# Performance work log

Measured on AMD Instinct MI355X. Metric: run time of the kernel, lower is better.

The kernel has to match this reference:

```python
import jax, jax.numpy as jnp
import numpy as np

B, T, C, HS = 64, 256, 2048, 128


def setup_inputs() -> dict:
    key = jax.random.key(0)
    k1, k2, k3, k4 = jax.random.split(key, 4)
    x = jax.random.normal(k1, (B, T, C), dtype=jnp.float32)
    # Dense(head_size, use_bias=False) kernels, scaled like glorot-ish init
    Wk = jax.random.normal(k2, (C, HS), dtype=jnp.float32) * (C ** -0.5)
    Wq = jax.random.normal(k3, (C, HS), dtype=jnp.float32) * (C ** -0.5)
    Wv = jax.random.normal(k4, (C, HS), dtype=jnp.float32) * (C ** -0.5)
    return {"x": x, "Wk": Wk, "Wq": Wq, "Wv": Wv}


def reference(x, Wk, Wq, Wv):
    Bn, Tn, Cn = x.shape
    k = jnp.einsum("btc,ch->bth", x, Wk)
    q = jnp.einsum("btc,ch->bth", x, Wq)
    v = jnp.einsum("btc,ch->bth", x, Wv)
    # faithful to source: scores = k @ q^T, scaled by C**-0.5 (input dim!)
    scores = jnp.einsum("bth,bsh->bts", k, q) * (Cn ** -0.5)
    causal = jnp.tril(jnp.ones((Tn, Tn), dtype=bool))  # [T, T]
    scores = jnp.where(causal, scores, -jnp.inf)
    weights = jax.nn.softmax(scores, axis=-1)
    return jnp.einsum("bts,bsh->bth", weights, v)
```

## Files before the change

### kernel.cpp

```cpp
#include <hip/hip_runtime.h>
#include <hip/hip_bf16.h>
#include <cstdint>
#include <cstddef>

#define B_  64
#define T_  256
#define C_  2048
#define HS_ 128
#define N_  384

typedef __bf16 bf16x8 __attribute__((ext_vector_type(8)));
typedef float  floatx4 __attribute__((ext_vector_type(4)));

__device__ __forceinline__ unsigned short f2bf_rne(float f) {
  union { float f; unsigned int u; } v; v.f = f;
  unsigned int r = v.u + 0x7fffu + ((v.u >> 16) & 1u);
  return (unsigned short)(r >> 16);
}
__device__ __forceinline__ unsigned short f2bf(float f) {
  union { float f; unsigned int u; } v; v.f = f;
  return (unsigned short)((v.u + 0x8000u) >> 16);
}

__global__ __launch_bounds__(256) void wt_kernel(
    const float* __restrict__ Wk, const float* __restrict__ Wq,
    const float* __restrict__ Wv, unsigned short* __restrict__ Wt) {
  __shared__ float tile[32][33];
  const int w  = blockIdx.z;
  const int c0 = blockIdx.x * 32;
  const int h0 = blockIdx.y * 32;
  const float* W = (w == 0) ? Wk : (w == 1) ? Wq : Wv;
  const int tx = threadIdx.x & 31, ty = threadIdx.x >> 5;
#pragma unroll
  for (int i = 0; i < 32; i += 8)
    tile[ty + i][tx] = W[(size_t)(c0 + ty + i) * HS_ + h0 + tx];
  __syncthreads();
#pragma unroll
  for (int i = 0; i < 32; i += 8) {
    int hh = ty + i, cc = tx;
    Wt[(size_t)(w * HS_ + h0 + hh) * C_ + c0 + cc] = f2bf_rne(tile[cc][hh]);
  }
}

__global__ __launch_bounds__(256, 2) void qkv_gemm(
    const float* __restrict__ X, const unsigned short* __restrict__ Wt,
    unsigned short* __restrict__ kqv, unsigned short* __restrict__ vT) {
  __shared__ unsigned short As[2][64 * 32];

  const int tid  = threadIdx.x;
  const int wave = tid >> 6, lane = tid & 63;
  const int quad = lane >> 4, l16 = lane & 15;

  const int m0    = blockIdx.x * 64;
  const int nbase = blockIdx.y * 192 + wave * 48;

  const int arow  = tid >> 3;
  const int acol4 = (tid & 7) * 4;

  const float* Xr0 = X + (size_t)(m0 + arow) * C_ + acol4;
  const float* Xr1 = X + (size_t)(m0 + arow + 32) * C_ + acol4;

  const unsigned short* Bp[3];
#pragma unroll
  for (int nt = 0; nt < 3; ++nt)
    Bp[nt] = Wt + (size_t)(nbase + nt * 16 + l16) * C_ + quad * 8;

  float4 a0 = *(const float4*)(Xr0);
  float4 a1 = *(const float4*)(Xr1);
  bf16x8 bcur[3];
#pragma unroll
  for (int nt = 0; nt < 3; ++nt) bcur[nt] = *(const bf16x8*)(Bp[nt]);

  floatx4 acc[4][3] = {};

  for (int k = 0; k < 64; ++k) {
    const int cur = k & 1;
    ushort4 u0, u1;
    u0.x = f2bf(a0.x); u0.y = f2bf(a0.y); u0.z = f2bf(a0.z); u0.w = f2bf(a0.w);
    u1.x = f2bf(a1.x); u1.y = f2bf(a1.y); u1.z = f2bf(a1.z); u1.w = f2bf(a1.w);
    *(ushort4*)&As[cur][arow * 32 + acol4]        = u0;
    *(ushort4*)&As[cur][(arow + 32) * 32 + acol4] = u1;
    __syncthreads();

    bf16x8 bnxt[3] = {bcur[0], bcur[1], bcur[2]};
    if (k < 63) {
      const int kn = (k + 1) * 32;
      a0 = *(const float4*)(Xr0 + kn);
      a1 = *(const float4*)(Xr1 + kn);
#pragma unroll
      for (int nt = 0; nt < 3; ++nt)
        bnxt[nt] = *(const bf16x8*)(Bp[nt] + kn);
    }

    bf16x8 af[4];
#pragma unroll
    for (int mt = 0; mt < 4; ++mt)
      af[mt] = *(const bf16x8*)&As[cur][(mt * 16 + l16) * 32 + quad * 8];
#pragma unroll
    for (int mt = 0; mt < 4; ++mt)
#pragma unroll
      for (int nt = 0; nt < 3; ++nt)
        acc[mt][nt] = __builtin_amdgcn_mfma_f32_16x16x32_bf16(
            af[mt], bcur[nt], acc[mt][nt], 0, 0, 0);
#pragma unroll
    for (int nt = 0; nt < 3; ++nt) bcur[nt] = bnxt[nt];
  }

#pragma unroll
  for (int mt = 0; mt < 4; ++mt)
#pragma unroll
    for (int nt = 0; nt < 3; ++nt) {
      const int n = nbase + nt * 16 + l16;
      const bool isv = (nbase + nt * 16) >= 256;
#pragma unroll
      for (int r = 0; r < 4; ++r) {
        int m = m0 + mt * 16 + quad * 4 + r;
        unsigned short us = f2bf(acc[mt][nt][r]);
        kqv[(size_t)m * N_ + n] = us;
        if (isv) {
          int bb = m >> 8, tt = m & 255;
          vT[(size_t)bb * HS_ * T_ + (size_t)(n - 256) * T_ + tt] = us;
        }
      }
    }
}

__global__ __launch_bounds__(256) void attn_kernel(
    const unsigned short* __restrict__ kqv, const unsigned short* __restrict__ vT,
    float* __restrict__ out) {
  constexpr int PS = 264;
  __shared__ unsigned short P[16 * PS];
  __shared__ float rsumw[4][16];

  const int tid  = threadIdx.x;
  const int p    = tid >> 6;
  const int lane = tid & 63;
  const int quad = lane >> 4, l16 = lane & 15;
  const int tt = blockIdx.x;
  const int b  = blockIdx.y;
  const int t0 = tt * 16;
  const float scale = 0.022097086912079612f;
  const unsigned short* kq = kqv + (size_t)b * T_ * N_;

  bf16x8 kf[4];
#pragma unroll
  for (int ks = 0; ks < 4; ++ks)
    kf[ks] = *(const bf16x8*)&kq[(size_t)(t0 + l16) * N_ + ks * 32 + quad * 8];

  if ((tt & 1) == 0 && p == ((tt + 1) & 3)) {
#pragma unroll
    for (int r = 0; r < 4; ++r)
      P[(quad * 4 + r) * PS + (tt + 1) * 16 + l16] = 0;
  }

  float rsum[4] = {0.f, 0.f, 0.f, 0.f};
  for (int st = p; st <= tt; st += 4) {
    floatx4 a = {};
#pragma unroll
    for (int ks = 0; ks < 4; ++ks) {
      bf16x8 qf = *(const bf16x8*)&kq[(size_t)(st * 16 + l16) * N_ + HS_ +
                                      ks * 32 + quad * 8];
      a = __builtin_amdgcn_mfma_f32_16x16x32_bf16(kf[ks], qf, a, 0, 0, 0);
    }
    const int scol = st * 16 + l16;
#pragma unroll
    for (int r = 0; r < 4; ++r) {
      int trow = t0 + quad * 4 + r;
      float pv = (scol <= trow) ? __expf(a[r] * scale) : 0.f;
      rsum[r] += pv;
      P[(quad * 4 + r) * PS + scol] = f2bf(pv);
    }
  }
#pragma unroll
  for (int m = 1; m < 16; m <<= 1)
#pragma unroll
    for (int r = 0; r < 4; ++r)
      rsum[r] += __shfl_xor(rsum[r], m, 64);
  if (l16 == 0) {
#pragma unroll
    for (int r = 0; r < 4; ++r) rsumw[p][quad * 4 + r] = rsum[r];
  }
  __syncthreads();

  const unsigned short* vb = vT + (size_t)b * HS_ * T_;
  const int h0 = p * 32;
  const int nks = (tt + 2) >> 1;
  floatx4 oacc[2] = {};
  for (int ks = 0; ks < nks; ++ks) {
    bf16x8 pa = *(const bf16x8*)&P[l16 * PS + ks * 32 + quad * 8];
#pragma unroll
    for (int nt = 0; nt < 2; ++nt) {
      bf16x8 bv = *(const bf16x8*)&vb[(size_t)(h0 + nt * 16 + l16) * T_ +
                                      ks * 32 + quad * 8];
      oacc[nt] = __builtin_amdgcn_mfma_f32_16x16x32_bf16(pa, bv, oacc[nt], 0, 0, 0);
    }
  }

  float tot[4];
#pragma unroll
  for (int r = 0; r < 4; ++r) {
    int row = quad * 4 + r;
    tot[r] = rsumw[0][row] + rsumw[1][row] + rsumw[2][row] + rsumw[3][row];
  }
  float* ob = out + ((size_t)b * T_ + t0) * HS_;
#pragma unroll
  for (int nt = 0; nt < 2; ++nt)
#pragma unroll
    for (int r = 0; r < 4; ++r) {
      int row = quad * 4 + r;
      ob[(size_t)row * HS_ + h0 + nt * 16 + l16] = oacc[nt][r] / tot[r];
    }
}

extern "C" void kernel_launch(void* const* d_in, const int* in_sizes, int n_in,
                              void* d_out, int out_size, void* d_ws, size_t ws_size,
                              hipStream_t stream) {
  const float* x  = (const float*)d_in[0];
  const float* Wk = (const float*)d_in[1];
  const float* Wq = (const float*)d_in[2];
  const float* Wv = (const float*)d_in[3];
  float* out = (float*)d_out;

  char* ws = (char*)d_ws;
  unsigned short* Wt  = (unsigned short*)(ws);
  unsigned short* kqv = (unsigned short*)(ws + 1572864);
  unsigned short* vT  = (unsigned short*)(ws + 1572864 + 12582912);

  hipLaunchKernelGGL(wt_kernel, dim3(64, 4, 3), dim3(256), 0, stream, Wk, Wq, Wv, Wt);
  hipLaunchKernelGGL(qkv_gemm, dim3(256, 2), dim3(256), 0, stream, x, Wt, kqv, vT);
  hipLaunchKernelGGL(attn_kernel, dim3(16, 64), dim3(256), 0, stream, kqv, vT, out);
}
```

Baseline: 253.8 us.

## Retile QKV GEMM to full-width 16-row blocks without LDS staging

The QKV projection GEMM now gives each block 16 rows of X and all 384 output columns, split as 96 columns per wave. Each X element is therefore read from memory only once instead of once per column block. The A fragment is loaded straight into registers and converted to bf16, with a two-step prefetch, so the shared-memory staging and its per-iteration barrier are gone. In exchange, every block streams the whole transposed weight matrix. That raises L2 traffic for the weights and lowers MFMA reuse per loaded B fragment.

```diff
diff --git a/kernel.cpp b/kernel.cpp
--- a/kernel.cpp
+++ b/kernel.cpp
@@ -42,87 +42,80 @@
   }
 }
 
-__global__ __launch_bounds__(256, 2) void qkv_gemm(
+__global__ __launch_bounds__(256, 3) void qkv_gemm(
     const float* __restrict__ X, const unsigned short* __restrict__ Wt,
     unsigned short* __restrict__ kqv, unsigned short* __restrict__ vT) {
-  __shared__ unsigned short As[2][64 * 32];
-
   const int tid  = threadIdx.x;
   const int wave = tid >> 6, lane = tid & 63;
   const int quad = lane >> 4, l16 = lane & 15;
 
-  const int m0    = blockIdx.x * 64;
-  const int nbase = blockIdx.y * 192 + wave * 48;
-
-  const int arow  = tid >> 3;
-  const int acol4 = (tid & 7) * 4;
-
-  const float* Xr0 = X + (size_t)(m0 + arow) * C_ + acol4;
-  const float* Xr1 = X + (size_t)(m0 + arow + 32) * C_ + acol4;
-
-  const unsigned short* Bp[3];
-#pragma unroll
-  for (int nt = 0; nt < 3; ++nt)
+  const int m0    = blockIdx.x * 16;
+  const int nbase = wave * 96;
+
+  const float* Xr = X + (size_t)(m0 + l16) * C_ + quad * 8;
+  const unsigned short* Bp[6];
+#pragma unroll
+  for (int nt = 0; nt < 6; ++nt)
     Bp[nt] = Wt + (size_t)(nbase + nt * 16 + l16) * C_ + quad * 8;
 
-  float4 a0 = *(const float4*)(Xr0);
-  float4 a1 = *(const float4*)(Xr1);
-  bf16x8 bcur[3];
-#pragma unroll
-  for (int nt = 0; nt < 3; ++nt) bcur[nt] = *(const bf16x8*)(Bp[nt]);
-
-  floatx4 acc[4][3] = {};
+  float4 ac0 = *(const float4*)(Xr);
+  float4 ac1 = *(const float4*)(Xr + 4);
+  float4 an0 = *(const float4*)(Xr + 32);
+  float4 an1 = *(const float4*)(Xr + 36);
+  bf16x8 bcur[6];
+#pragma unroll
+  for (int nt = 0; nt < 6; ++nt) bcur[nt] = *(const bf16x8*)(Bp[nt]);
+
+  floatx4 acc[6] = {};
 
   for (int k = 0; k < 64; ++k) {
-    const int cur = k & 1;
-    ushort4 u0, u1;
-    u0.x = f2bf(a0.x); u0.y = f2bf(a0.y); u0.z = f2bf(a0.z); u0.w = f2bf(a0.w);
-    u1.x = f2bf(a1.x); u1.y = f2bf(a1.y); u1.z = f2bf(a1.z); u1.w = f2bf(a1.w);
-    *(ushort4*)&As[cur][arow * 32 + acol4]        = u0;
-    *(ushort4*)&As[cur][(arow + 32) * 32 + acol4] = u1;
-    __syncthreads();
-
-    bf16x8 bnxt[3] = {bcur[0], bcur[1], bcur[2]};
+    bf16x8 bnxt[6];
+#pragma unroll
+    for (int nt = 0; nt < 6; ++nt) bnxt[nt] = bcur[nt];
+    float4 am0 = an0, am1 = an1;
     if (k < 63) {
-      const int kn = (k + 1) * 32;
-      a0 = *(const float4*)(Xr0 + kn);
-      a1 = *(const float4*)(Xr1 + kn);
-#pragma unroll
-      for (int nt = 0; nt < 3; ++nt)
-        bnxt[nt] = *(const bf16x8*)(Bp[nt] + kn);
-    }
-
-    bf16x8 af[4];
-#pragma unroll
-    for (int mt = 0; mt < 4; ++mt)
-      af[mt] = *(const bf16x8*)&As[cur][(mt * 16 + l16) * 32 + quad * 8];
-#pragma unroll
-    for (int mt = 0; mt < 4; ++mt)
-#pragma unroll
-      for (int nt = 0; nt < 3; ++nt)
-        acc[mt][nt] = __builtin_amdgcn_mfma_f32_16x16x32_bf16(
-            af[mt], bcur[nt], acc[mt][nt], 0, 0, 0);
-#pragma unroll
-    for (int nt = 0; nt < 3; ++nt) bcur[nt] = bnxt[nt];
-  }
-
-#pragma unroll
-  for (int mt = 0; mt < 4; ++mt)
-#pragma unroll
-    for (int nt = 0; nt < 3; ++nt) {
-      const int n = nbase + nt * 16 + l16;
-      const bool isv = (nbase + nt * 16) >= 256;
-#pragma unroll
-      for (int r = 0; r < 4; ++r) {
-        int m = m0 + mt * 16 + quad * 4 + r;
-        unsigned short us = f2bf(acc[mt][nt][r]);
-        kqv[(size_t)m * N_ + n] = us;
-        if (isv) {
-          int bb = m >> 8, tt = m & 255;
-          vT[(size_t)bb * HS_ * T_ + (size_t)(n - 256) * T_ + tt] = us;
-        }
+      const int kb = (k + 1) * 32;
+#pragma unroll
+      for (int nt = 0; nt < 6; ++nt)
+        bnxt[nt] = *(const bf16x8*)(Bp[nt] + kb);
+    }
+    if (k < 62) {
+      const int kf = (k + 2) * 32;
+      am0 = *(const float4*)(Xr + kf);
+      am1 = *(const float4*)(Xr + kf + 4);
+    }
+
+    union { ushort4 u4[2]; bf16x8 v; } pk;
+    pk.u4[0].x = f2bf(ac0.x); pk.u4[0].y = f2bf(ac0.y);
+    pk.u4[0].z = f2bf(ac0.z); pk.u4[0].w = f2bf(ac0.w);
+    pk.u4[1].x = f2bf(ac1.x); pk.u4[1].y = f2bf(ac1.y);
+    pk.u4[1].z = f2bf(ac1.z); pk.u4[1].w = f2bf(ac1.w);
+
+#pragma unroll
+    for (int nt = 0; nt < 6; ++nt)
+      acc[nt] = __builtin_amdgcn_mfma_f32_16x16x32_bf16(
+          pk.v, bcur[nt], acc[nt], 0, 0, 0);
+
+    ac0 = an0; ac1 = an1; an0 = am0; an1 = am1;
+#pragma unroll
+    for (int nt = 0; nt < 6; ++nt) bcur[nt] = bnxt[nt];
+  }
+
+#pragma unroll
+  for (int nt = 0; nt < 6; ++nt) {
+    const int n   = nbase + nt * 16 + l16;
+    const bool isv = (nbase + nt * 16) >= 256;
+#pragma unroll
+    for (int r = 0; r < 4; ++r) {
+      int m = m0 + quad * 4 + r;
+      unsigned short us = f2bf(acc[nt][r]);
+      kqv[(size_t)m * N_ + n] = us;
+      if (isv) {
+        int bb = m >> 8, tt = m & 255;
+        vT[(size_t)bb * HS_ * T_ + (size_t)(n - 256) * T_ + tt] = us;
       }
     }
+  }
 }
 
 __global__ __launch_bounds__(256) void attn_kernel(
@@ -227,6 +220,6 @@
   unsigned short* vT  = (unsigned short*)(ws + 1572864 + 12582912);
 
   hipLaunchKernelGGL(wt_kernel, dim3(64, 4, 3), dim3(256), 0, stream, Wk, Wq, Wv, Wt);
-  hipLaunchKernelGGL(qkv_gemm, dim3(256, 2), dim3(256), 0, stream, x, Wt, kqv, vT);
+  hipLaunchKernelGGL(qkv_gemm, dim3(1024), dim3(256), 0, stream, x, Wt, kqv, vT);
   hipLaunchKernelGGL(attn_kernel, dim3(16, 64), dim3(256), 0, stream, kqv, vT, out);
 }
```

New measurement: 419.5 us. +65.3%, slower.
